# Kernel tuning notes

Hardware: AMD Instinct MI355X
Metric: run time of the kernel (lower is better)

## Reference

```python
import jax, jax.numpy as jnp
import numpy as np

D = 512      # model_channels
H = 4        # heads
L = 4        # num_transfomers_layers
DK = D // H
EPS = 1e-5


def inorm(x):
    # nn.InstanceNorm1d(d_model) applied to (bs, seq, d_model): normalizes over
    # the last (d_model) axis per token, no affine params.
    m = jnp.mean(x, axis=-1, keepdims=True)
    v = jnp.var(x, axis=-1, keepdims=True)
    return (x - m) * jax.lax.rsqrt(v + EPS)


def mha(xq, xkv, w, b, mask):
    # w: [4, D, D] (q,k,v,out), b: [4, D]; mask: [bs,S,S] (1 = masked)
    bs, S, _ = xq.shape
    q = (xq @ w[0] + b[0]).reshape(bs, S, H, DK).transpose(0, 2, 1, 3)
    k = (xkv @ w[1] + b[1]).reshape(bs, S, H, DK).transpose(0, 2, 1, 3)
    v = (xkv @ w[2] + b[2]).reshape(bs, S, H, DK).transpose(0, 2, 1, 3)
    scores = jnp.einsum('bhqd,bhkd->bhqk', q, k) / jnp.sqrt(jnp.float32(DK))
    scores = jnp.where(mask[:, None] == 1, jnp.float32(-1e9), scores)
    attn = jax.nn.softmax(scores, axis=-1)
    out = jnp.einsum('bhqk,bhkd->bhqd', attn, v)
    out = out.transpose(0, 2, 1, 3).reshape(bs, S, D)
    return out @ w[3] + b[3]


def setup_inputs() -> dict:
    key = jax.random.key(0)
    ks = jax.random.split(key, 24)
    bs, S = 16, 512
    sc = 0.02
    inp = {
        'x': jax.random.normal(ks[0], (bs, S, 18), jnp.float32),
        'cond': jax.random.normal(ks[1], (bs, S, 89), jnp.float32),
        'door_mask': jax.random.randint(ks[2], (bs, S, S), 0, 2, jnp.int32),
        'self_mask': jax.random.randint(ks[3], (bs, S, S), 0, 2, jnp.int32),
        'gen_mask': jax.random.randint(ks[4], (bs, S, S), 0, 2, jnp.int32),
        # attention params: [L, 3 branches (door,self,gen), 4 projs (q,k,v,out)]
        'attn_w': jax.random.normal(ks[5], (L, 3, 4, D, D), jnp.float32) * sc,
        'attn_b': jnp.zeros((L, 3, 4, D), jnp.float32),
        'ff_w1': jax.random.normal(ks[6], (L, D, 2 * D), jnp.float32) * sc,
        'ff_b1': jnp.zeros((L, 2 * D), jnp.float32),
        'ff_w2': jax.random.normal(ks[7], (L, 2 * D, D), jnp.float32) * sc,
        'ff_b2': jnp.zeros((L, D), jnp.float32),
        'in_w': jax.random.normal(ks[8], (18, D), jnp.float32) * sc,
        'in_b': jnp.zeros((D,), jnp.float32),
        'cond_w': jax.random.normal(ks[9], (89, D), jnp.float32) * sc,
        'cond_b': jnp.zeros((D,), jnp.float32),
        'out1_w': jax.random.normal(ks[10], (D, D), jnp.float32) * sc,
        'out1_b': jnp.zeros((D,), jnp.float32),
        'out2_w': jax.random.normal(ks[11], (D, D // 2), jnp.float32) * sc,
        'out2_b': jnp.zeros((D // 2,), jnp.float32),
        'out3_w': jax.random.normal(ks[12], (D // 2, 2), jnp.float32) * sc,
        'out3_b': jnp.zeros((2,), jnp.float32),
    }
    return inp


def reference(x, cond, door_mask, self_mask, gen_mask,
              attn_w, attn_b, ff_w1, ff_b1, ff_w2, ff_b2,
              in_w, in_b, cond_w, cond_b,
              out1_w, out1_b, out2_w, out2_b, out3_w, out3_b):
    h = (x @ in_w + in_b) + (cond @ cond_w + cond_b)  # [bs,S,D]
    for l in range(L):
        h2 = inorm(h)
        h = (h
             + mha(h2, h2, attn_w[l, 0], attn_b[l, 0], door_mask)
             + mha(h2, h2, attn_w[l, 1], attn_b[l, 1], self_mask)
             + mha(h2, h2, attn_w[l, 2], attn_b[l, 2], gen_mask))
        h2 = inorm(h)
        h = h + jax.nn.relu(h2 @ ff_w1[l] + ff_b1[l]) @ ff_w2[l] + ff_b2[l]
    out = jax.nn.relu(h @ out1_w + out1_b)
    out = jax.nn.relu(out @ out2_w + out2_b)
    out = out @ out3_w + out3_b  # [bs,S,2]
    return out
```

## Files before the change

kernel.cpp:

```cpp
#include <hip/hip_runtime.h>
#include <hip/hip_bf16.h>

#define DEV static __device__ __forceinline__

typedef __attribute__((ext_vector_type(8))) short bfx8;
typedef __attribute__((ext_vector_type(4))) float f32x4;
typedef __attribute__((ext_vector_type(4))) unsigned short us4;

DEV unsigned short f2bf(float f){
  unsigned u = __builtin_bit_cast(unsigned, f);
  u += 0x7fffu + ((u >> 16) & 1u);
  return (unsigned short)(u >> 16);
}
DEV float bf2f(unsigned short h){
  unsigned u = ((unsigned)h) << 16;
  return __builtin_bit_cast(float, u);
}
DEV void gld16(const void* g, void* l){
  __builtin_amdgcn_global_load_lds((const __attribute__((address_space(1))) void*)g,
                                   (__attribute__((address_space(3))) void*)l, 16, 0, 0);
}
DEV f32x4 mfma16(bfx8 a, bfx8 b, f32x4 c){
  return __builtin_amdgcn_mfma_f32_16x16x32_bf16(a, b, c, 0, 0, 0);
}

__global__ __launch_bounds__(256, 2)
void wconv_kernel(const float* __restrict__ attn_w, const float* __restrict__ ff_w1,
                  const float* __restrict__ ff_w2, const float* __restrict__ out1_w,
                  const float* __restrict__ out2_w,
                  unsigned short* __restrict__ bqkv, unsigned short* __restrict__ bout,
                  unsigned short* __restrict__ bff1, unsigned short* __restrict__ bff2,
                  unsigned short* __restrict__ bo1, unsigned short* __restrict__ bo2)
{
  __shared__ float ts[64][65];
  const int z = blockIdx.z;
  const float* src; unsigned short* dst; int K, N, stride;
  if (z < 48){
    int l = z / 12, br = (z % 12) >> 2, p = z & 3;
    src = attn_w + (size_t)z * 262144; K = 512; N = 512;
    if (p < 3){ dst = bqkv + (size_t)l * 4608 * 512 + (size_t)(br * 3 + p) * 262144; stride = 512; }
    else      { dst = bout + (size_t)l * 512 * 1536 + (size_t)br * 512;              stride = 1536; }
  } else if (z < 52){
    int l = z - 48; src = ff_w1 + (size_t)l * 524288; K = 512; N = 1024;
    dst = bff1 + (size_t)l * 524288; stride = 512;
  } else if (z < 56){
    int l = z - 52; src = ff_w2 + (size_t)l * 524288; K = 1024; N = 512;
    dst = bff2 + (size_t)l * 524288; stride = 1024;
  } else if (z == 56){
    src = out1_w; K = 512; N = 512; dst = bo1; stride = 512;
  } else {
    src = out2_w; K = 512; N = 256; dst = bo2; stride = 512;
  }
  const int n0 = blockIdx.x << 6, k0 = blockIdx.y << 6;
  if (n0 >= N || k0 >= K) return;
  const int tx = threadIdx.x & 63, ty = threadIdx.x >> 6;
  #pragma unroll
  for (int i = 0; i < 16; ++i){
    int row = (ty << 4) + i;
    ts[row][tx] = src[(size_t)(k0 + row) * N + n0 + tx];
  }
  __syncthreads();
  #pragma unroll
  for (int i = 0; i < 16; ++i){
    int row = (ty << 4) + i;
    dst[(size_t)(n0 + row) * stride + k0 + tx] = f2bf(ts[tx][row]);
  }
}

__global__ __launch_bounds__(256, 4)
void mpack_kernel(const int* __restrict__ m0, const int* __restrict__ m1,
                  const int* __restrict__ m2, unsigned long long* __restrict__ mp)
{
  const int row = (blockIdx.x << 2) + (threadIdx.x >> 6);
  const int lane = threadIdx.x & 63;
  const int* src = (row < 8192) ? (m0 + (size_t)row * 512)
                 : (row < 16384 ? (m1 + (size_t)(row - 8192) * 512)
                                : (m2 + (size_t)(row - 16384) * 512));
  #pragma unroll
  for (int c = 0; c < 8; ++c){
    const int v = src[(c << 6) + lane];
    const unsigned long long b = __ballot(v != 0);
    if (lane == c) mp[(size_t)row * 8 + c] = b;
  }
}

__global__ __launch_bounds__(256, 4)
void embed_kernel(const float* __restrict__ x, const float* __restrict__ cond,
                  const float* __restrict__ in_w, const float* __restrict__ in_b,
                  const float* __restrict__ cond_w, const float* __restrict__ cond_b,
                  float* __restrict__ h)
{
  __shared__ float xs[18];
  __shared__ float cs[89];
  const int m = blockIdx.x;
  const int tid = threadIdx.x;
  if (tid < 18) xs[tid] = x[(size_t)m * 18 + tid];
  if (tid >= 32 && tid < 121) cs[tid - 32] = cond[(size_t)m * 89 + (tid - 32)];
  __syncthreads();
  #pragma unroll
  for (int hf = 0; hf < 2; ++hf){
    const int c = tid + (hf << 8);
    float a = in_b[c] + cond_b[c];
    #pragma unroll
    for (int k = 0; k < 18; ++k) a += xs[k] * in_w[k * 512 + c];
    for (int k = 0; k < 89; ++k) a += cs[k] * cond_w[k * 512 + c];
    h[(size_t)m * 512 + c] = a;
  }
}

__global__ __launch_bounds__(256, 4)
void inorm_kernel(const float* __restrict__ in, unsigned short* __restrict__ ob)
{
  const int wid = (blockIdx.x << 2) + (threadIdx.x >> 6);
  const int lane = threadIdx.x & 63;
  const float* row = in + (size_t)wid * 512;
  const float4 v0 = *(const float4*)(row + (lane << 2));
  const float4 v1 = *(const float4*)(row + 256 + (lane << 2));
  float s = v0.x + v0.y + v0.z + v0.w + v1.x + v1.y + v1.z + v1.w;
  float q = v0.x*v0.x + v0.y*v0.y + v0.z*v0.z + v0.w*v0.w
          + v1.x*v1.x + v1.y*v1.y + v1.z*v1.z + v1.w*v1.w;
  #pragma unroll
  for (int sh = 1; sh < 64; sh <<= 1){
    s += __shfl_xor(s, sh, 64);
    q += __shfl_xor(q, sh, 64);
  }
  const float mean = s * (1.f / 512.f);
  const float var = q * (1.f / 512.f) - mean * mean;
  const float rs = rsqrtf(var + 1e-5f);
  us4 o0, o1;
  o0[0] = f2bf((v0.x - mean) * rs); o0[1] = f2bf((v0.y - mean) * rs);
  o0[2] = f2bf((v0.z - mean) * rs); o0[3] = f2bf((v0.w - mean) * rs);
  o1[0] = f2bf((v1.x - mean) * rs); o1[1] = f2bf((v1.y - mean) * rs);
  o1[2] = f2bf((v1.z - mean) * rs); o1[3] = f2bf((v1.w - mean) * rs);
  *(us4*)(ob + (size_t)wid * 512 + (lane << 2)) = o0;
  *(us4*)(ob + (size_t)wid * 512 + 256 + (lane << 2)) = o1;
}

__global__ void f2b_kernel(const float* __restrict__ in, unsigned short* __restrict__ ob, int n)
{
  const int i = (blockIdx.x * 256 + threadIdx.x) << 2;
  if (i >= n) return;
  const float4 v = *(const float4*)(in + i);
  us4 o; o[0] = f2bf(v.x); o[1] = f2bf(v.y); o[2] = f2bf(v.z); o[3] = f2bf(v.w);
  *(us4*)(ob + i) = o;
}

template<int MODE>
__global__ __launch_bounds__(256, 2)
void gemm_bt(const unsigned short* __restrict__ A, const unsigned short* __restrict__ B,
             const float* __restrict__ bias, float* __restrict__ Cf,
             unsigned short* __restrict__ Cb, unsigned short* __restrict__ qkp,
             unsigned short* __restrict__ vtp, int M, int N, int K)
{
  __shared__ unsigned short As[128 * 64];
  __shared__ unsigned short Bs[128 * 64];
  const int tid = threadIdx.x;
  const int w = tid >> 6, lane = tid & 63;
  const int wm = w >> 1, wn = w & 1;
  const int lr = lane & 15, lh = lane >> 4;
  const int m0 = blockIdx.x << 7, n0 = blockIdx.y << 7;
  const int rA = lane >> 3;
  const int cA = (lane & 7) << 3;

  f32x4 acc[4][4];
  #pragma unroll
  for (int i = 0; i < 4; ++i)
    #pragma unroll
    for (int j = 0; j < 4; ++j) acc[i][j] = (f32x4)0.f;

  const int nkt = K >> 6;
  auto stage = [&](int kt){
    #pragma unroll
    for (int c = 0; c < 4; ++c){
      const int r = (c << 5) + (w << 3) + rA;
      gld16(A + (size_t)(m0 + r) * K + (kt << 6) + cA,
            (char*)As + ((c << 5) + (w << 3)) * 128);
      gld16(B + (size_t)(n0 + r) * K + (kt << 6) + cA,
            (char*)Bs + ((c << 5) + (w << 3)) * 128);
    }
  };
  stage(0);
  for (int kt = 0; kt < nkt; ++kt){
    __syncthreads();
    #pragma unroll
    for (int kk = 0; kk < 2; ++kk){
      bfx8 af[4], bg[4];
      #pragma unroll
      for (int i = 0; i < 4; ++i)
        af[i] = *(const bfx8*)(As + ((wm << 6) + (i << 4) + lr) * 64 + (kk << 5) + (lh << 3));
      #pragma unroll
      for (int j = 0; j < 4; ++j)
        bg[j] = *(const bfx8*)(Bs + ((wn << 6) + (j << 4) + lr) * 64 + (kk << 5) + (lh << 3));
      #pragma unroll
      for (int i = 0; i < 4; ++i)
        #pragma unroll
        for (int j = 0; j < 4; ++j)
          acc[i][j] = mfma16(af[i], bg[j], acc[i][j]);
    }
    __syncthreads();
    if (kt + 1 < nkt) stage(kt + 1);
  }
  #pragma unroll
  for (int i = 0; i < 4; ++i){
    const int row = m0 + (wm << 6) + (i << 4) + (lh << 2);
    #pragma unroll
    for (int j = 0; j < 4; ++j){
      const int col = n0 + (wn << 6) + (j << 4) + lr;
      if constexpr (MODE == 1){
        const float bv = bias ? bias[col] : 0.f;
        #pragma unroll
        for (int r = 0; r < 4; ++r){
          float v = acc[i][j][r] + bv;
          v = fmaxf(v, 0.f);
          Cb[(size_t)(row + r) * N + col] = f2bf(v);
        }
      } else if constexpr (MODE == 2){
        const float bv = bias ? bias[col] : 0.f;
        #pragma unroll
        for (int r = 0; r < 4; ++r){
          const size_t idx = (size_t)(row + r) * N + col;
          Cf[idx] += acc[i][j][r] + bv;
        }
      } else {
        const int br = col / 1536;
        const int rem = col - br * 1536;
        const int p = rem >> 9;
        const int c = rem & 511;
        const float bv = bias ? bias[(size_t)((br << 2) + p) * 512 + c] : 0.f;
        if (p < 2){
          #pragma unroll
          for (int r = 0; r < 4; ++r)
            qkp[((size_t)((br << 1) + p) * 8192 + row + r) * 512 + c] = f2bf(acc[i][j][r] + bv);
        } else {
          const int b_ = row >> 9, s0 = row & 511;
          const int hi = c >> 7, dk = c & 127;
          us4 pk;
          #pragma unroll
          for (int r = 0; r < 4; ++r) pk[r] = f2bf(acc[i][j][r] + bv);
          *(us4*)(vtp + (((size_t)(br * 16 + b_) * 4 + hi) * 128 + dk) * 512 + s0) = pk;
        }
      }
    }
  }
}

__global__ __launch_bounds__(256, 2)
void attn_kernel(const unsigned short* __restrict__ qk, const unsigned short* __restrict__ vt,
                 const unsigned* __restrict__ mp, unsigned short* __restrict__ outp)
{
  __shared__ unsigned short KV[2][4096];
  __shared__ unsigned short Pl[4][16 * 40];
  __shared__ unsigned Mk[64 * 17];
  const int tid = threadIdx.x;
  const int w = tid >> 6, lane = tid & 63;
  const int lr = lane & 15, lh = lane >> 4;
  const int id = blockIdx.x;
  const int pair = (id & 7) * 192 / 8 + ((id >> 3) >> 3);
  const int qt = (id >> 3) & 7;
  const int br = pair >> 6, bh = pair & 63;
  const int b = bh >> 2, h = bh & 3;
  const int q0 = (qt << 6) + (w << 4);

  const unsigned short* qbase = qk + ((size_t)(br * 2 + 0) * 8192 + (size_t)b * 512) * 512 + h * 128;
  const unsigned short* kbase = qk + ((size_t)(br * 2 + 1) * 8192 + (size_t)b * 512) * 512 + h * 128;
  const unsigned short* vbase = vt + ((size_t)(br * 16 + b) * 4 + h) * 128 * 512;
  const unsigned* mrow = mp + ((size_t)br * 8192 + (size_t)b * 512 + (qt << 6)) * 16;

  for (int idx = tid; idx < 1024; idx += 256){
    const int rw = idx >> 4, wd = idx & 15;
    Mk[rw * 17 + wd] = mrow[rw * 16 + wd];
  }

  bfx8 aq[4];
  #pragma unroll
  for (int t = 0; t < 4; ++t)
    aq[t] = *(const bfx8*)(qbase + (size_t)(q0 + lr) * 512 + (t << 5) + (lh << 3));

  f32x4 sc[16][2];
  const float scale = 0.08838834764831845f;

  auto stageK = [&](int kt){
    char* dst = (char*)KV[kt & 1];
    #pragma unroll
    for (int c2 = 0; c2 < 2; ++c2){
      const int trow = (c2 << 4) + (w << 2) + (lane >> 4);
      const int g = (lane & 15) ^ (trow & 7);
      gld16(kbase + (size_t)((kt << 5) + trow) * 512 + (g << 3),
            dst + ((c2 << 4) + (w << 2)) * 256);
    }
  };
  auto stageV = [&](int kt){
    char* dst = (char*)KV[kt & 1];
    #pragma unroll
    for (int c2 = 0; c2 < 2; ++c2){
      const int drow = (c2 << 6) + (w << 4) + (lane >> 2);
      const int g = (lane & 3) ^ (drow & 3);
      gld16(vbase + (size_t)drow * 512 + (kt << 5) + (g << 3),
            dst + ((c2 << 6) + (w << 4)) * 64);
    }
  };

  stageK(0);
  for (int kt = 0; kt < 16; ++kt){
    __syncthreads();
    if (kt < 15) stageK(kt + 1);
    const unsigned short* Ksb = KV[kt & 1];
    #pragma unroll
    for (int j = 0; j < 2; ++j){
      const int rk = (j << 4) + lr;
      f32x4 a2 = (f32x4)0.f;
      #pragma unroll
      for (int t = 0; t < 4; ++t){
        const int s = ((t << 2) + lh) ^ (rk & 7);
        bfx8 bk = *(const bfx8*)(Ksb + rk * 128 + (s << 3));
        a2 = mfma16(aq[t], bk, a2);
      }
      #pragma unroll
      for (int r = 0; r < 4; ++r){
        const int qloc = (w << 4) + (lh << 2) + r;
        const unsigned mword = Mk[qloc * 17 + kt];
        const int bit = (mword >> ((j << 4) + lr)) & 1;
        sc[kt][j][r] = bit ? -1e9f : a2[r] * scale;
      }
    }
  }

  float mx[4] = {-3e38f, -3e38f, -3e38f, -3e38f};
  #pragma unroll
  for (int kt = 0; kt < 16; ++kt)
    #pragma unroll
    for (int j = 0; j < 2; ++j)
      #pragma unroll
      for (int r = 0; r < 4; ++r) mx[r] = fmaxf(mx[r], sc[kt][j][r]);
  #pragma unroll
  for (int s = 1; s < 16; s <<= 1)
    #pragma unroll
    for (int r = 0; r < 4; ++r) mx[r] = fmaxf(mx[r], __shfl_xor(mx[r], s, 64));
  float sm[4] = {0.f, 0.f, 0.f, 0.f};
  #pragma unroll
  for (int kt = 0; kt < 16; ++kt)
    #pragma unroll
    for (int j = 0; j < 2; ++j)
      #pragma unroll
      for (int r = 0; r < 4; ++r){
        const float pv = __expf(sc[kt][j][r] - mx[r]);
        sc[kt][j][r] = pv;
        sm[r] += pv;
      }
  #pragma unroll
  for (int s = 1; s < 16; s <<= 1)
    #pragma unroll
    for (int r = 0; r < 4; ++r) sm[r] += __shfl_xor(sm[r], s, 64);
  float linv[4];
  #pragma unroll
  for (int r = 0; r < 4; ++r) linv[r] = 1.f / sm[r];

  f32x4 ao[8];
  #pragma unroll
  for (int j = 0; j < 8; ++j) ao[j] = (f32x4)0.f;
  unsigned short* pw = Pl[w];
  __syncthreads();
  stageV(0);
  for (int kt = 0; kt < 16; ++kt){
    __syncthreads();
    if (kt < 15) stageV(kt + 1);
    #pragma unroll
    for (int j = 0; j < 2; ++j)
      #pragma unroll
      for (int r = 0; r < 4; ++r)
        pw[((lh << 2) + r) * 40 + (j << 4) + lr] = f2bf(sc[kt][j][r] * linv[r]);
    bfx8 pa = *(const bfx8*)(pw + lr * 40 + (lh << 3));
    const unsigned short* Vsb = KV[kt & 1];
    #pragma unroll
    for (int j = 0; j < 8; ++j){
      const int dd = (j << 4) + lr;
      const int s = lh ^ (dd & 3);
      bfx8 bv = *(const bfx8*)(Vsb + dd * 32 + (s << 3));
      ao[j] = mfma16(pa, bv, ao[j]);
    }
  }
  const size_t obase = (size_t)(b * 512) * 1536 + br * 512 + h * 128;
  #pragma unroll
  for (int j = 0; j < 8; ++j){
    const int d = (j << 4) + lr;
    #pragma unroll
    for (int r = 0; r < 4; ++r){
      const int q = q0 + (lh << 2) + r;
      outp[obase + (size_t)q * 1536 + d] = f2bf(ao[j][r]);
    }
  }
}

__global__ __launch_bounds__(256, 4)
void out3_kernel(const unsigned short* __restrict__ t2, const float* __restrict__ w,
                 const float* __restrict__ b2, float* __restrict__ outp)
{
  const int row = (blockIdx.x << 2) + (threadIdx.x >> 6);
  const int lane = threadIdx.x & 63;
  const unsigned short* rp = t2 + (size_t)row * 256 + (lane << 2);
  float a0 = 0.f, a1 = 0.f;
  #pragma unroll
  for (int k = 0; k < 4; ++k){
    const float v = bf2f(rp[k]);
    const int kk = (lane << 2) + k;
    a0 += v * w[kk * 2 + 0];
    a1 += v * w[kk * 2 + 1];
  }
  #pragma unroll
  for (int s = 1; s < 64; s <<= 1){
    a0 += __shfl_xor(a0, s, 64);
    a1 += __shfl_xor(a1, s, 64);
  }
  if (lane == 0){
    outp[(size_t)row * 2 + 0] = a0 + b2[0];
    outp[(size_t)row * 2 + 1] = a1 + b2[1];
  }
}

extern "C" void kernel_launch(void* const* d_in, const int* in_sizes, int n_in,
                              void* d_out, int out_size, void* d_ws, size_t ws_size,
                              hipStream_t stream)
{
  const float* x      = (const float*)d_in[0];
  const float* cond   = (const float*)d_in[1];
  const int*   mdoor  = (const int*)d_in[2];
  const int*   mself  = (const int*)d_in[3];
  const int*   mgen   = (const int*)d_in[4];
  const float* attn_w = (const float*)d_in[5];
  const float* attn_b = (const float*)d_in[6];
  const float* ff_w1  = (const float*)d_in[7];
  const float* ff_b1  = (const float*)d_in[8];
  const float* ff_w2  = (const float*)d_in[9];
  const float* ff_b2  = (const float*)d_in[10];
  const float* in_w   = (const float*)d_in[11];
  const float* in_b   = (const float*)d_in[12];
  const float* cond_w = (const float*)d_in[13];
  const float* cond_b = (const float*)d_in[14];
  const float* out1_w = (const float*)d_in[15];
  const float* out1_b = (const float*)d_in[16];
  const float* out2_w = (const float*)d_in[17];
  const float* out2_b = (const float*)d_in[18];
  const float* out3_w = (const float*)d_in[19];
  const float* out3_b = (const float*)d_in[20];

  char* p = (char*)d_ws;
  auto carve = [&](size_t bytes) -> char* {
    char* r = p; p += (bytes + 255) & ~(size_t)255; return r;
  };
  float*          h    = (float*)carve(8192ull * 512 * 4);
  unsigned short* h2   = (unsigned short*)carve(8192ull * 512 * 2);
  unsigned short* bqkv = (unsigned short*)carve(4ull * 4608 * 512 * 2);
  unsigned short* bout = (unsigned short*)carve(4ull * 512 * 1536 * 2);
  unsigned short* bff1 = (unsigned short*)carve(4ull * 1024 * 512 * 2);
  unsigned short* bff2 = (unsigned short*)carve(4ull * 512 * 1024 * 2);
  unsigned short* bo1  = (unsigned short*)carve(512ull * 512 * 2);
  unsigned short* bo2  = (unsigned short*)carve(256ull * 512 * 2);
  unsigned short* qkb  = (unsigned short*)carve(6ull * 8192 * 512 * 2);
  unsigned short* vtb  = (unsigned short*)carve(3ull * 16 * 4 * 128 * 512 * 2);
  unsigned short* att  = (unsigned short*)carve(8192ull * 1536 * 2);
  unsigned short* t    = (unsigned short*)carve(8192ull * 1024 * 2);
  unsigned short* t2   = (unsigned short*)carve(8192ull * 256 * 2);
  unsigned long long* mpk = (unsigned long long*)carve(24576ull * 8 * 8);
  float* outf = (float*)d_out;

  wconv_kernel<<<dim3(16, 16, 58), 256, 0, stream>>>(attn_w, ff_w1, ff_w2, out1_w, out2_w,
                                                     bqkv, bout, bff1, bff2, bo1, bo2);
  mpack_kernel<<<dim3(6144), 256, 0, stream>>>(mdoor, mself, mgen, mpk);
  embed_kernel<<<dim3(8192), 256, 0, stream>>>(x, cond, in_w, in_b, cond_w, cond_b, h);
  for (int l = 0; l < 4; ++l){
    inorm_kernel<<<dim3(2048), 256, 0, stream>>>(h, h2);
    gemm_bt<3><<<dim3(64, 36), 256, 0, stream>>>(h2, bqkv + (size_t)l * 4608 * 512,
        attn_b + (size_t)l * 6144, nullptr, nullptr, qkb, vtb, 8192, 4608, 512);
    attn_kernel<<<dim3(1536), 256, 0, stream>>>(qkb, vtb, (const unsigned*)mpk, att);
    gemm_bt<2><<<dim3(64, 4), 256, 0, stream>>>(att, bout + (size_t)l * 512 * 1536,
        nullptr, h, nullptr, nullptr, nullptr, 8192, 512, 1536);
    inorm_kernel<<<dim3(2048), 256, 0, stream>>>(h, h2);
    gemm_bt<1><<<dim3(64, 8), 256, 0, stream>>>(h2, bff1 + (size_t)l * 1024 * 512,
        ff_b1 + (size_t)l * 1024, nullptr, t, nullptr, nullptr, 8192, 1024, 512);
    gemm_bt<2><<<dim3(64, 4), 256, 0, stream>>>(t, bff2 + (size_t)l * 512 * 1024,
        ff_b2 + (size_t)l * 512, h, nullptr, nullptr, nullptr, 8192, 512, 1024);
  }
  f2b_kernel<<<dim3(4096), 256, 0, stream>>>(h, h2, 8192 * 512);
  gemm_bt<1><<<dim3(64, 4), 256, 0, stream>>>(h2, bo1, out1_b, nullptr, att, nullptr, nullptr, 8192, 512, 512);
  gemm_bt<1><<<dim3(64, 2), 256, 0, stream>>>(att, bo2, out2_b, nullptr, t2, nullptr, nullptr, 8192, 256, 512);
  out3_kernel<<<dim3(2048), 256, 0, stream>>>(t2, out3_w, out3_b, outf);
}
```

Before: 1.298 ms.

## Rewrite attention as single-pass online softmax with triple-buffered K/V staging

```diff
diff --git a/kernel.cpp b/kernel.cpp
--- a/kernel.cpp
+++ b/kernel.cpp
@@ -23,6 +23,9 @@
 DEV f32x4 mfma16(bfx8 a, bfx8 b, f32x4 c){
   return __builtin_amdgcn_mfma_f32_16x16x32_bf16(a, b, c, 0, 0, 0);
 }
+
+#define BAR() do{ asm volatile("" ::: "memory"); __builtin_amdgcn_s_barrier(); \
+                  asm volatile("" ::: "memory"); }while(0)
 
 __global__ __launch_bounds__(256, 2)
 void wconv_kernel(const float* __restrict__ attn_w, const float* __restrict__ ff_w1,
@@ -90,21 +93,33 @@
                   const float* __restrict__ cond_w, const float* __restrict__ cond_b,
                   float* __restrict__ h)
 {
-  __shared__ float xs[18];
-  __shared__ float cs[89];
-  const int m = blockIdx.x;
+  __shared__ float xs[8][18];
+  __shared__ float cs[8][89];
+  const int m0 = blockIdx.x << 3;
   const int tid = threadIdx.x;
-  if (tid < 18) xs[tid] = x[(size_t)m * 18 + tid];
-  if (tid >= 32 && tid < 121) cs[tid - 32] = cond[(size_t)m * 89 + (tid - 32)];
+  for (int i = tid; i < 144; i += 256) xs[i / 18][i % 18] = x[(size_t)m0 * 18 + i];
+  for (int i = tid; i < 712; i += 256) cs[i / 89][i % 89] = cond[(size_t)m0 * 89 + i];
   __syncthreads();
   #pragma unroll
   for (int hf = 0; hf < 2; ++hf){
     const int c = tid + (hf << 8);
-    float a = in_b[c] + cond_b[c];
-    #pragma unroll
-    for (int k = 0; k < 18; ++k) a += xs[k] * in_w[k * 512 + c];
-    for (int k = 0; k < 89; ++k) a += cs[k] * cond_w[k * 512 + c];
-    h[(size_t)m * 512 + c] = a;
+    const float bsum = in_b[c] + cond_b[c];
+    float a[8];
+    #pragma unroll
+    for (int mi = 0; mi < 8; ++mi) a[mi] = bsum;
+    #pragma unroll
+    for (int k = 0; k < 18; ++k){
+      const float wv = in_w[k * 512 + c];
+      #pragma unroll
+      for (int mi = 0; mi < 8; ++mi) a[mi] += xs[mi][k] * wv;
+    }
+    for (int k = 0; k < 89; ++k){
+      const float wv = cond_w[k * 512 + c];
+      #pragma unroll
+      for (int mi = 0; mi < 8; ++mi) a[mi] += cs[mi][k] * wv;
+    }
+    #pragma unroll
+    for (int mi = 0; mi < 8; ++mi) h[(size_t)(m0 + mi) * 512 + c] = a[mi];
   }
 }
 
@@ -217,10 +232,8 @@
       } else if constexpr (MODE == 2){
         const float bv = bias ? bias[col] : 0.f;
         #pragma unroll
-        for (int r = 0; r < 4; ++r){
-          const size_t idx = (size_t)(row + r) * N + col;
-          Cf[idx] += acc[i][j][r] + bv;
-        }
+        for (int r = 0; r < 4; ++r)
+          Cf[(size_t)(row + r) * N + col] += acc[i][j][r] + bv;
       } else {
         const int br = col / 1536;
         const int rem = col - br * 1536;
@@ -244,141 +257,148 @@
   }
 }
 
-__global__ __launch_bounds__(256, 2)
+__global__ __launch_bounds__(512, 4)
 void attn_kernel(const unsigned short* __restrict__ qk, const unsigned short* __restrict__ vt,
                  const unsigned* __restrict__ mp, unsigned short* __restrict__ outp)
 {
-  __shared__ unsigned short KV[2][4096];
-  __shared__ unsigned short Pl[4][16 * 40];
-  __shared__ unsigned Mk[64 * 17];
+  __shared__ unsigned short KV[3][8192];
+  __shared__ unsigned short Pl[8][16 * 40];
+  __shared__ unsigned Mk[8][16 * 17];
   const int tid = threadIdx.x;
   const int w = tid >> 6, lane = tid & 63;
   const int lr = lane & 15, lh = lane >> 4;
   const int id = blockIdx.x;
-  const int pair = (id & 7) * 192 / 8 + ((id >> 3) >> 3);
-  const int qt = (id >> 3) & 7;
-  const int br = pair >> 6, bh = pair & 63;
+  const int wg = (id & 7) * 96 + (id >> 3);
+  const int qt = wg & 3, head = wg >> 2;
+  const int br = head >> 6, bh = head & 63;
   const int b = bh >> 2, h = bh & 3;
-  const int q0 = (qt << 6) + (w << 4);
+  const int q0 = (qt << 7) + (w << 4);
 
   const unsigned short* qbase = qk + ((size_t)(br * 2 + 0) * 8192 + (size_t)b * 512) * 512 + h * 128;
   const unsigned short* kbase = qk + ((size_t)(br * 2 + 1) * 8192 + (size_t)b * 512) * 512 + h * 128;
   const unsigned short* vbase = vt + ((size_t)(br * 16 + b) * 4 + h) * 128 * 512;
-  const unsigned* mrow = mp + ((size_t)br * 8192 + (size_t)b * 512 + (qt << 6)) * 16;
-
-  for (int idx = tid; idx < 1024; idx += 256){
+  const unsigned* mrow = mp + ((size_t)br * 8192 + (size_t)b * 512 + q0) * 16;
+
+  unsigned* mk = Mk[w];
+  #pragma unroll
+  for (int u = 0; u < 4; ++u){
+    const int idx = (lane << 2) + u;
     const int rw = idx >> 4, wd = idx & 15;
-    Mk[rw * 17 + wd] = mrow[rw * 16 + wd];
-  }
+    mk[rw * 17 + wd] = mrow[rw * 16 + wd];
+  }
+  asm volatile("s_waitcnt lgkmcnt(0)" ::: "memory");
+  __builtin_amdgcn_sched_barrier(0);
 
   bfx8 aq[4];
   #pragma unroll
   for (int t = 0; t < 4; ++t)
     aq[t] = *(const bfx8*)(qbase + (size_t)(q0 + lr) * 512 + (t << 5) + (lh << 3));
 
-  f32x4 sc[16][2];
+  const int krow = (w << 2) + (lane >> 4);
+  const int kg = (lane & 15) ^ (krow & 7);
+  const int vrow = (w << 4) + (lane >> 2);
+  const int vg = (lane & 3) ^ ((vrow & 3) ^ ((vrow >> 2) & 3));
+  auto stageKt = [&](int kt, int buf){
+    gld16(kbase + ((size_t)((kt << 5) + krow) << 9) + (kg << 3),
+          (char*)&KV[buf][w << 9]);
+    gld16(vbase + ((size_t)vrow << 9) + (kt << 5) + (vg << 3),
+          (char*)&KV[buf][4096 + (w << 9)]);
+  };
+
   const float scale = 0.08838834764831845f;
-
-  auto stageK = [&](int kt){
-    char* dst = (char*)KV[kt & 1];
-    #pragma unroll
-    for (int c2 = 0; c2 < 2; ++c2){
-      const int trow = (c2 << 4) + (w << 2) + (lane >> 4);
-      const int g = (lane & 15) ^ (trow & 7);
-      gld16(kbase + (size_t)((kt << 5) + trow) * 512 + (g << 3),
-            dst + ((c2 << 4) + (w << 2)) * 256);
-    }
-  };
-  auto stageV = [&](int kt){
-    char* dst = (char*)KV[kt & 1];
-    #pragma unroll
-    for (int c2 = 0; c2 < 2; ++c2){
-      const int drow = (c2 << 6) + (w << 4) + (lane >> 2);
-      const int g = (lane & 3) ^ (drow & 3);
-      gld16(vbase + (size_t)drow * 512 + (kt << 5) + (g << 3),
-            dst + ((c2 << 6) + (w << 4)) * 64);
-    }
-  };
-
-  stageK(0);
+  f32x4 ao[8];
+  #pragma unroll
+  for (int j = 0; j < 8; ++j) ao[j] = (f32x4)0.f;
+  float m[4]  = {-3e38f, -3e38f, -3e38f, -3e38f};
+  float lp[4] = {0.f, 0.f, 0.f, 0.f};
+  unsigned short* pw = Pl[w];
+
+  stageKt(0, 0); stageKt(1, 1);
+  int bcur = 0;
   for (int kt = 0; kt < 16; ++kt){
-    __syncthreads();
-    if (kt < 15) stageK(kt + 1);
-    const unsigned short* Ksb = KV[kt & 1];
+    if (kt < 15) asm volatile("s_waitcnt vmcnt(2)" ::: "memory");
+    else         asm volatile("s_waitcnt vmcnt(0)" ::: "memory");
+    BAR();
+    if (kt < 14){
+      const int bst = (bcur == 0) ? 2 : bcur - 1;
+      stageKt(kt + 2, bst);
+    }
+    const unsigned short* Kb = &KV[bcur][0];
+    const unsigned short* Vb = &KV[bcur][4096];
+
+    f32x4 st[2];
     #pragma unroll
     for (int j = 0; j < 2; ++j){
       const int rk = (j << 4) + lr;
       f32x4 a2 = (f32x4)0.f;
+      __builtin_amdgcn_s_setprio(1);
       #pragma unroll
       for (int t = 0; t < 4; ++t){
         const int s = ((t << 2) + lh) ^ (rk & 7);
-        bfx8 bk = *(const bfx8*)(Ksb + rk * 128 + (s << 3));
+        bfx8 bk = *(const bfx8*)&Kb[rk * 128 + (s << 3)];
         a2 = mfma16(aq[t], bk, a2);
       }
+      __builtin_amdgcn_s_setprio(0);
       #pragma unroll
       for (int r = 0; r < 4; ++r){
-        const int qloc = (w << 4) + (lh << 2) + r;
-        const unsigned mword = Mk[qloc * 17 + kt];
+        const unsigned mword = mk[((lh << 2) + r) * 17 + kt];
         const int bit = (mword >> ((j << 4) + lr)) & 1;
-        sc[kt][j][r] = bit ? -1e9f : a2[r] * scale;
+        st[j][r] = bit ? -1e9f : a2[r] * scale;
       }
     }
-  }
-
-  float mx[4] = {-3e38f, -3e38f, -3e38f, -3e38f};
-  #pragma unroll
-  for (int kt = 0; kt < 16; ++kt)
+
+    float tm[4];
+    #pragma unroll
+    for (int r = 0; r < 4; ++r) tm[r] = fmaxf(st[0][r], st[1][r]);
+    #pragma unroll
+    for (int s = 1; s < 16; s <<= 1)
+      #pragma unroll
+      for (int r = 0; r < 4; ++r) tm[r] = fmaxf(tm[r], __shfl_xor(tm[r], s, 64));
+    bool need = false;
+    #pragma unroll
+    for (int r = 0; r < 4; ++r) need |= (tm[r] > m[r] + 8.f);
+    if (__any(need)){
+      #pragma unroll
+      for (int r = 0; r < 4; ++r){
+        const float mn = fmaxf(m[r], tm[r]);
+        const float f = __expf(m[r] - mn);
+        m[r] = mn; lp[r] *= f;
+        #pragma unroll
+        for (int j = 0; j < 8; ++j) ao[j][r] *= f;
+      }
+    }
     #pragma unroll
     for (int j = 0; j < 2; ++j)
       #pragma unroll
-      for (int r = 0; r < 4; ++r) mx[r] = fmaxf(mx[r], sc[kt][j][r]);
-  #pragma unroll
-  for (int s = 1; s < 16; s <<= 1)
-    #pragma unroll
-    for (int r = 0; r < 4; ++r) mx[r] = fmaxf(mx[r], __shfl_xor(mx[r], s, 64));
-  float sm[4] = {0.f, 0.f, 0.f, 0.f};
-  #pragma unroll
-  for (int kt = 0; kt < 16; ++kt)
-    #pragma unroll
-    for (int j = 0; j < 2; ++j)
-      #pragma unroll
       for (int r = 0; r < 4; ++r){
-        const float pv = __expf(sc[kt][j][r] - mx[r]);
-        sc[kt][j][r] = pv;
-        sm[r] += pv;
+        const float p = __expf(st[j][r] - m[r]);
+        lp[r] += p;
+        pw[((lh << 2) + r) * 40 + (j << 4) + lr] = f2bf(p);
       }
-  #pragma unroll
-  for (int s = 1; s < 16; s <<= 1)
-    #pragma unroll
-    for (int r = 0; r < 4; ++r) sm[r] += __shfl_xor(sm[r], s, 64);
-  float linv[4];
-  #pragma unroll
-  for (int r = 0; r < 4; ++r) linv[r] = 1.f / sm[r];
-
-  f32x4 ao[8];
-  #pragma unroll
-  for (int j = 0; j < 8; ++j) ao[j] = (f32x4)0.f;
-  unsigned short* pw = Pl[w];
-  __syncthreads();
-  stageV(0);
-  for (int kt = 0; kt < 16; ++kt){
-    __syncthreads();
-    if (kt < 15) stageV(kt + 1);
-    #pragma unroll
-    for (int j = 0; j < 2; ++j)
-      #pragma unroll
-      for (int r = 0; r < 4; ++r)
-        pw[((lh << 2) + r) * 40 + (j << 4) + lr] = f2bf(sc[kt][j][r] * linv[r]);
+    asm volatile("s_waitcnt lgkmcnt(0)" ::: "memory");
+    __builtin_amdgcn_sched_barrier(0);
     bfx8 pa = *(const bfx8*)(pw + lr * 40 + (lh << 3));
-    const unsigned short* Vsb = KV[kt & 1];
+
+    __builtin_amdgcn_s_setprio(1);
     #pragma unroll
     for (int j = 0; j < 8; ++j){
       const int dd = (j << 4) + lr;
-      const int s = lh ^ (dd & 3);
-      bfx8 bv = *(const bfx8*)(Vsb + dd * 32 + (s << 3));
+      const int s = lh ^ ((dd & 3) ^ ((dd >> 2) & 3));
+      bfx8 bv = *(const bfx8*)&Vb[dd * 32 + (s << 3)];
       ao[j] = mfma16(pa, bv, ao[j]);
     }
-  }
+    __builtin_amdgcn_s_setprio(0);
+    asm volatile("" ::: "memory");
+    bcur = (bcur == 2) ? 0 : bcur + 1;
+  }
+
+  #pragma unroll
+  for (int s = 1; s < 16; s <<= 1)
+    #pragma unroll
+    for (int r = 0; r < 4; ++r) lp[r] += __shfl_xor(lp[r], s, 64);
+  float linv[4];
+  #pragma unroll
+  for (int r = 0; r < 4; ++r) linv[r] = 1.f / lp[r];
   const size_t obase = (size_t)(b * 512) * 1536 + br * 512 + h * 128;
   #pragma unroll
   for (int j = 0; j < 8; ++j){
@@ -386,7 +406,7 @@
     #pragma unroll
     for (int r = 0; r < 4; ++r){
       const int q = q0 + (lh << 2) + r;
-      outp[obase + (size_t)q * 1536 + d] = f2bf(ao[j][r]);
+      outp[obase + (size_t)q * 1536 + d] = f2bf(ao[j][r] * linv[r]);
     }
   }
 }
@@ -466,12 +486,12 @@
   wconv_kernel<<<dim3(16, 16, 58), 256, 0, stream>>>(attn_w, ff_w1, ff_w2, out1_w, out2_w,
                                                      bqkv, bout, bff1, bff2, bo1, bo2);
   mpack_kernel<<<dim3(6144), 256, 0, stream>>>(mdoor, mself, mgen, mpk);
-  embed_kernel<<<dim3(8192), 256, 0, stream>>>(x, cond, in_w, in_b, cond_w, cond_b, h);
+  embed_kernel<<<dim3(1024), 256, 0, stream>>>(x, cond, in_w, in_b, cond_w, cond_b, h);
   for (int l = 0; l < 4; ++l){
     inorm_kernel<<<dim3(2048), 256, 0, stream>>>(h, h2);
     gemm_bt<3><<<dim3(64, 36), 256, 0, stream>>>(h2, bqkv + (size_t)l * 4608 * 512,
         attn_b + (size_t)l * 6144, nullptr, nullptr, qkb, vtb, 8192, 4608, 512);
-    attn_kernel<<<dim3(1536), 256, 0, stream>>>(qkb, vtb, (const unsigned*)mpk, att);
+    attn_kernel<<<dim3(768), 512, 0, stream>>>(qkb, vtb, (const unsigned*)mpk, att);
     gemm_bt<2><<<dim3(64, 4), 256, 0, stream>>>(att, bout + (size_t)l * 512 * 1536,
         nullptr, h, nullptr, nullptr, nullptr, 8192, 512, 1536);
     inorm_kernel<<<dim3(2048), 256, 0, stream>>>(h, h2);
```

Measured after the change: 1.221 ms. 5.9% less time.
